# Optimization experiments

Hardware: AMD Instinct MI355X
Metric: run time of the kernel (lower is better)

Reference implementation:

```python
import jax, jax.numpy as jnp
import numpy as np
import math

B, T, D, H, L = 64, 255, 512, 8, 8
CODEBOOK = 512
V = CODEBOOK + 3  # bos/eos/pad
COND_DIM = 512
MAX_LEN = 256
HD = D // H


def _layernorm(x, g, b, eps=1e-5):
    mu = jnp.mean(x, axis=-1, keepdims=True)
    var = jnp.mean(jnp.square(x - mu), axis=-1, keepdims=True)
    return (x - mu) * jax.lax.rsqrt(var + eps) * g + b


def setup_inputs() -> dict:
    key = jax.random.key(0)
    ks = jax.random.split(key, 24)
    s = 0.02
    d = {
        'tokens': jax.random.randint(ks[0], (B, T), 0, V),
        'cond': jax.random.normal(ks[1], (B, COND_DIM), jnp.float32),
        'emb': jax.random.normal(ks[2], (V, D), jnp.float32) * s,  # tied token_emb / head weight
        'pos_emb': jax.random.normal(ks[3], (1, MAX_LEN, D), jnp.float32) * s,
        'cond_w1': jax.random.normal(ks[4], (COND_DIM, D), jnp.float32) * s,
        'cond_b1': jnp.zeros((D,), jnp.float32),
        'cond_w2': jax.random.normal(ks[5], (D, D), jnp.float32) * s,
        'cond_b2': jnp.zeros((D,), jnp.float32),
        'ln1_g': jnp.ones((L, D), jnp.float32),
        'ln1_b': jnp.zeros((L, D), jnp.float32),
        'qkv_w': jax.random.normal(ks[6], (L, D, 3 * D), jnp.float32) * s,
        'qkv_b': jnp.zeros((L, 3 * D), jnp.float32),
        'proj_w': jax.random.normal(ks[7], (L, D, D), jnp.float32) * s,
        'proj_b': jnp.zeros((L, D), jnp.float32),
        'ln2_g': jnp.ones((L, D), jnp.float32),
        'ln2_b': jnp.zeros((L, D), jnp.float32),
        'mlp_w1': jax.random.normal(ks[8], (L, D, 4 * D), jnp.float32) * s,
        'mlp_b1': jnp.zeros((L, 4 * D), jnp.float32),
        'mlp_w2': jax.random.normal(ks[9], (L, 4 * D, D), jnp.float32) * s,
        'mlp_b2': jnp.zeros((L, D), jnp.float32),
        'lnf_g': jnp.ones((D,), jnp.float32),
        'lnf_b': jnp.zeros((D,), jnp.float32),
    }
    return d


def reference(tokens, cond, emb, pos_emb, cond_w1, cond_b1, cond_w2, cond_b2,
              ln1_g, ln1_b, qkv_w, qkv_b, proj_w, proj_b,
              ln2_g, ln2_b, mlp_w1, mlp_b1, mlp_w2, mlp_b2, lnf_g, lnf_b):
    b, t = tokens.shape
    h = emb[tokens] + pos_emb[:, :t, :]                              # [B,T,D]
    c = jax.nn.silu(cond @ cond_w1 + cond_b1) @ cond_w2 + cond_b2    # [B,D]
    h = jnp.concatenate([c[:, None, :], h], axis=1)                  # [B,S,D]
    S = t + 1
    causal = jnp.tril(jnp.ones((S, S), bool))
    scale = 1.0 / math.sqrt(HD)
    for i in range(L):
        x = _layernorm(h, ln1_g[i], ln1_b[i])
        qkv = (x @ qkv_w[i] + qkv_b[i]).reshape(b, S, 3, H, HD).transpose(2, 0, 3, 1, 4)
        q, k, v = qkv[0], qkv[1], qkv[2]                             # [B,H,S,hd]
        a = jnp.einsum('bhsd,bhtd->bhst', q, k) * scale
        a = jnp.where(causal, a, -jnp.inf)
        a = jax.nn.softmax(a, axis=-1)
        o = jnp.einsum('bhst,bhtd->bhsd', a, v).transpose(0, 2, 1, 3).reshape(b, S, D)
        h = h + o @ proj_w[i] + proj_b[i]
        x = _layernorm(h, ln2_g[i], ln2_b[i])
        h = h + jax.nn.gelu(x @ mlp_w1[i] + mlp_b1[i], approximate=False) @ mlp_w2[i] + mlp_b2[i]
    h = _layernorm(h, lnf_g, lnf_b)
    return (h @ emb.T)[:, 1:, :]                                     # [B,T,V]
```

## Files before the change

kernel.cpp:

```cpp
#include <hip/hip_runtime.h>
#include <hip/hip_bf16.h>

typedef __attribute__((ext_vector_type(8))) short bf16x8;
typedef __attribute__((ext_vector_type(4))) float f32x4;
typedef __attribute__((ext_vector_type(4))) unsigned short u16x4;
typedef __attribute__((ext_vector_type(8))) unsigned short u16x8;
typedef unsigned short u16;

#define DEV static __device__ __forceinline__

DEV float bf2f(u16 u) {
  union { unsigned int i; float f; } c; c.i = ((unsigned int)u) << 16; return c.f;
}
DEV u16 f2bf(float f) {
  union { float f; unsigned int i; } c; c.f = f;
  unsigned int i = c.i;
  i += 0x7FFFu + ((i >> 16) & 1u);
  return (u16)(i >> 16);
}

DEV void gload_lds16(const void* g, void* l) {
  __builtin_amdgcn_global_load_lds((const __attribute__((address_space(1))) void*)g,
                                   (__attribute__((address_space(3))) void*)l, 16, 0, 0);
}

DEV f32x4 mfma16(bf16x8 a, bf16x8 b, f32x4 c) {
  return __builtin_amdgcn_mfma_f32_16x16x32_bf16(a, b, c, 0, 0, 0);
}

template<int N> DEV void vwait() { asm volatile("s_waitcnt vmcnt(%0)" :: "n"(N) : "memory"); }

DEV float gelu(float x) {
  float t2 = __builtin_fmaf(0.044715f * x * x, x, x);
  float e = __expf(1.5957691216f * t2);
  float th = 1.f - 2.f / (e + 1.f);
  return 0.5f * x * (1.f + th);
}

__global__ __launch_bounds__(256) void ktranspose(const float* __restrict__ in, u16* __restrict__ out,
                                                  int K, int N) {
  __shared__ u16 tile[32][33];
  const float* src = in + (size_t)blockIdx.z * K * N;
  u16* dst = out + (size_t)blockIdx.z * K * N;
  const int n0 = blockIdx.x * 32, k0 = blockIdx.y * 32;
  const int tx = threadIdx.x, ty = threadIdx.y;
#pragma unroll
  for (int i = ty; i < 32; i += 8) tile[i][tx] = f2bf(src[(size_t)(k0 + i) * N + n0 + tx]);
  __syncthreads();
#pragma unroll
  for (int i = ty; i < 32; i += 8) dst[(size_t)(n0 + i) * K + k0 + tx] = tile[tx][i];
}

__global__ __launch_bounds__(256) void kcvt(const float* __restrict__ in, u16* __restrict__ out, int n) {
  int i = blockIdx.x * 256 + threadIdx.x;
  if (i < n) out[i] = f2bf(in[i]);
}

__global__ __launch_bounds__(256) void kcond(const float* __restrict__ cond, const float* __restrict__ w1,
                                             const float* __restrict__ b1, const float* __restrict__ w2,
                                             const float* __restrict__ b2, float* __restrict__ h) {
  __shared__ float xr[512];
  __shared__ float t1[512];
  const int b = blockIdx.x, tid = threadIdx.x;
  for (int i = tid; i < 512; i += 256) xr[i] = cond[b * 512 + i];
  __syncthreads();
  for (int j = tid; j < 512; j += 256) {
    float acc = b1[j];
    for (int k = 0; k < 512; ++k) acc += xr[k] * w1[k * 512 + j];
    t1[j] = acc / (1.f + __expf(-acc));
  }
  __syncthreads();
  for (int j = tid; j < 512; j += 256) {
    float acc = b2[j];
    for (int k = 0; k < 512; ++k) acc += t1[k] * w2[k * 512 + j];
    h[(size_t)b * 256 * 512 + j] = acc;
  }
}

__global__ __launch_bounds__(256) void kembed(const int* __restrict__ tok, const float* __restrict__ emb,
                                              const float* __restrict__ pos, float* __restrict__ h) {
  const int idx = blockIdx.x;
  const int b = idx / 255, t = idx % 255;
  const int c = threadIdx.x * 2;
  const int tk = tok[idx];
  float2 ev = *(const float2*)(emb + (size_t)tk * 512 + c);
  float2 pv = *(const float2*)(pos + (size_t)t * 512 + c);
  float2 r;
  r.x = ev.x + pv.x;
  r.y = ev.y + pv.y;
  *(float2*)(h + ((size_t)b * 256 + 1 + t) * 512 + c) = r;
}

__global__ __launch_bounds__(256) void kln(const float* __restrict__ hin, const float* __restrict__ g,
                                           const float* __restrict__ bt, u16* __restrict__ out) {
  const int row = blockIdx.x * 4 + (threadIdx.x >> 6), lane = threadIdx.x & 63;
  const float4* x = (const float4*)(hin + (size_t)row * 512);
  float4 v0 = x[lane], v1 = x[lane + 64];
  float s1 = v0.x + v0.y + v0.z + v0.w + v1.x + v1.y + v1.z + v1.w;
  float s2 = v0.x * v0.x + v0.y * v0.y + v0.z * v0.z + v0.w * v0.w +
             v1.x * v1.x + v1.y * v1.y + v1.z * v1.z + v1.w * v1.w;
#pragma unroll
  for (int off = 1; off < 64; off <<= 1) { s1 += __shfl_xor(s1, off); s2 += __shfl_xor(s2, off); }
  float mu = s1 * (1.f / 512.f);
  float var = s2 * (1.f / 512.f) - mu * mu;
  float rs = rsqrtf(var + 1e-5f);
  const int c0 = lane * 4;
  float4 g0 = *(const float4*)(g + c0), g1 = *(const float4*)(g + 256 + c0);
  float4 b0 = *(const float4*)(bt + c0), b1 = *(const float4*)(bt + 256 + c0);
  u16x4 o0, o1;
  o0[0] = f2bf((v0.x - mu) * rs * g0.x + b0.x);
  o0[1] = f2bf((v0.y - mu) * rs * g0.y + b0.y);
  o0[2] = f2bf((v0.z - mu) * rs * g0.z + b0.z);
  o0[3] = f2bf((v0.w - mu) * rs * g0.w + b0.w);
  o1[0] = f2bf((v1.x - mu) * rs * g1.x + b1.x);
  o1[1] = f2bf((v1.y - mu) * rs * g1.y + b1.y);
  o1[2] = f2bf((v1.z - mu) * rs * g1.z + b1.z);
  o1[3] = f2bf((v1.w - mu) * rs * g1.w + b1.w);
  *(u16x4*)(out + (size_t)row * 512 + c0) = o0;
  *(u16x4*)(out + (size_t)row * 512 + 256 + c0) = o1;
}

template<int MODE>
__global__ __launch_bounds__(256, 2) void kgemm3(const u16* __restrict__ A, const u16* __restrict__ Bt,
                                                 const float* __restrict__ bias, void* __restrict__ Cout,
                                                 int M, int N, int K) {
  __shared__ __align__(16) u16 As[3][4096];
  __shared__ __align__(16) u16 Bs[3][4096];
  const int tid = threadIdx.x;
  const int lane = tid & 63;
  const int wr = tid >> 7, wc = (tid >> 6) & 1;
  const int m0 = blockIdx.x * 128, n0 = blockIdx.y * 128;
  const int nkt = K >> 5;
  const size_t Kb = (size_t)K * 2;

  const int srow = tid >> 2;
  const int schunk = tid & 3;
  const int sc = schunk ^ ((srow >> 1) & 3);
  const int d1 = tid * 16, d2 = tid * 16 + 4096;
  int brA = n0 + srow, brB = n0 + srow + 64;
  if (MODE == 3) { brA = min(brA, N - 1); brB = min(brB, N - 1); }
  const char* Ab = (const char*)A;
  const char* Bb = (const char*)Bt;
  const size_t a0 = (size_t)(m0 + srow) * Kb + sc * 16;
  const size_t a1 = (size_t)(m0 + srow + 64) * Kb + sc * 16;
  const size_t b0 = (size_t)brA * Kb + sc * 16;
  const size_t b1 = (size_t)brB * Kb + sc * 16;

  f32x4 acc[4][4];
#pragma unroll
  for (int i = 0; i < 4; ++i)
#pragma unroll
    for (int j = 0; j < 4; ++j) acc[i][j] = f32x4{0.f, 0.f, 0.f, 0.f};

#pragma unroll
  for (int t = 0; t < 2; ++t) {
    const size_t ko = (size_t)t * 64;
    gload_lds16(Ab + a0 + ko, (char*)As[t] + d1);
    gload_lds16(Ab + a1 + ko, (char*)As[t] + d2);
    gload_lds16(Bb + b0 + ko, (char*)Bs[t] + d1);
    gload_lds16(Bb + b1 + ko, (char*)Bs[t] + d2);
  }
  asm volatile("s_waitcnt vmcnt(4)" ::: "memory");
  __builtin_amdgcn_s_barrier();
  __builtin_amdgcn_sched_barrier(0);

  const int kchunk = (((lane >> 4) ^ ((lane >> 1) & 3)) << 4);
  const int arow = wr * 64 + (lane & 15);
  const int brow = wc * 64 + (lane & 15);

  for (int kt = 0; kt < nkt; ++kt) {
    const int bufc = kt % 3;
    const bool deep = (kt + 2 < nkt);
    if (deep) {
      const int bufn = (kt + 2) % 3;
      const size_t ko = (size_t)(kt + 2) * 64;
      gload_lds16(Ab + a0 + ko, (char*)As[bufn] + d1);
      gload_lds16(Ab + a1 + ko, (char*)As[bufn] + d2);
      gload_lds16(Bb + b0 + ko, (char*)Bs[bufn] + d1);
      gload_lds16(Bb + b1 + ko, (char*)Bs[bufn] + d2);
    }
    const char* Ap = (const char*)As[bufc];
    const char* Bp = (const char*)Bs[bufc];
    bf16x8 aF[4], bF[4];
#pragma unroll
    for (int mt = 0; mt < 4; ++mt) aF[mt] = *(const bf16x8*)(Ap + (arow + mt * 16) * 64 + kchunk);
#pragma unroll
    for (int nt = 0; nt < 4; ++nt) bF[nt] = *(const bf16x8*)(Bp + (brow + nt * 16) * 64 + kchunk);
#pragma unroll
    for (int mt = 0; mt < 4; ++mt)
#pragma unroll
      for (int nt = 0; nt < 4; ++nt)
        acc[mt][nt] = mfma16(aF[mt], bF[nt], acc[mt][nt]);
    if (deep) {
      asm volatile("s_waitcnt vmcnt(4)" ::: "memory");
    } else {
      asm volatile("s_waitcnt vmcnt(0)" ::: "memory");
    }
    __builtin_amdgcn_s_barrier();
    __builtin_amdgcn_sched_barrier(0);
  }

  float bv[4];
#pragma unroll
  for (int nt = 0; nt < 4; ++nt) {
    int col = n0 + wc * 64 + nt * 16 + (lane & 15);
    bv[nt] = (MODE == 3) ? 0.f : bias[col];
  }

  if (MODE == 0 || MODE == 1) {
    u16* C = (u16*)Cout;
#pragma unroll
    for (int mt = 0; mt < 4; ++mt)
#pragma unroll
      for (int r = 0; r < 4; ++r) {
        int row = m0 + wr * 64 + mt * 16 + (lane >> 4) * 4 + r;
        u16* cp = C + (size_t)row * N + n0 + wc * 64 + (lane & 15);
#pragma unroll
        for (int nt = 0; nt < 4; ++nt) {
          float v = acc[mt][nt][r] + bv[nt];
          if (MODE == 1) v = gelu(v);
          cp[nt * 16] = f2bf(v);
        }
      }
  } else if (MODE == 2) {
    float* hC = (float*)Cout;
#pragma unroll
    for (int mt = 0; mt < 4; ++mt)
#pragma unroll
      for (int r = 0; r < 4; ++r) {
        int row = m0 + wr * 64 + mt * 16 + (lane >> 4) * 4 + r;
        float* hp = hC + (size_t)row * N + n0 + wc * 64 + (lane & 15);
#pragma unroll
        for (int nt = 0; nt < 4; ++nt) hp[nt * 16] += acc[mt][nt][r] + bv[nt];
      }
  } else {
    float* C = (float*)Cout;
#pragma unroll
    for (int mt = 0; mt < 4; ++mt)
#pragma unroll
      for (int r = 0; r < 4; ++r) {
        int row = m0 + wr * 64 + mt * 16 + (lane >> 4) * 4 + r;
        int s = row & 255;
        if (s == 0) continue;
        int bb = row >> 8;
        float* cp = C + ((size_t)bb * 255 + (s - 1)) * 515 + n0 + wc * 64 + (lane & 15);
#pragma unroll
        for (int nt = 0; nt < 4; ++nt) {
          int col = n0 + wc * 64 + nt * 16 + (lane & 15);
          if (col < 515) cp[nt * 16] = acc[mt][nt][r];
        }
      }
  }
}

template<int MODE, int FM>
__global__ __launch_bounds__(512, 2) void kgemm8(const u16* __restrict__ A, const u16* __restrict__ Bt,
                                                 const float* __restrict__ bias, void* __restrict__ Cout,
                                                 int M, int N, int K) {
  constexpr int BM = FM * 32;
  constexpr int ABYTES = BM * 128;
  constexpr int BBYTES = 256 * 128;
  constexpr int AH = ABYTES / 2, BH = BBYTES / 2;
  constexpr int ALD = AH / 8192;
  constexpr int BOFF = 2 * ABYTES;
  __shared__ __align__(16) char shm[2 * ABYTES + 2 * BBYTES];

  const int tid = threadIdx.x;
  const int lane = tid & 63;
  const int wid = tid >> 6;
  const int wr = wid >> 2;
  const int wc = wid & 3;
  const int fr = lane & 15, fq = lane >> 4;
  const int axor = (fr & 7) << 4;
  const int m0 = blockIdx.x * BM, n0 = blockIdx.y * 256;
  const int nkt = K >> 6;
  const int Kb = K * 2;
  const char* Ab = (const char*)A;
  const char* Bb = (const char*)Bt;

  unsigned aOff[2][ALD], bOff[2][2];
#pragma unroll
  for (int h = 0; h < 2; ++h) {
#pragma unroll
    for (int j = 0; j < ALD; ++j) {
      int d = h * AH + j * 8192 + tid * 16;
      int row = d >> 7, pc = (d >> 4) & 7;
      aOff[h][j] = (unsigned)((m0 + row) * Kb + ((pc ^ (row & 7)) << 4));
    }
#pragma unroll
    for (int j = 0; j < 2; ++j) {
      int d = h * BH + j * 8192 + tid * 16;
      int row = d >> 7, pc = (d >> 4) & 7;
      bOff[h][j] = (unsigned)((n0 + row) * Kb + ((pc ^ (row & 7)) << 4));
    }
  }

  auto stA = [&](int kt, int h, int b) {
#pragma unroll
    for (int j = 0; j < ALD; ++j)
      gload_lds16(Ab + (size_t)aOff[h][j] + (size_t)kt * 128,
                  shm + b * ABYTES + h * AH + j * 8192 + tid * 16);
  };
  auto stB = [&](int kt, int h, int b) {
#pragma unroll
    for (int j = 0; j < 2; ++j)
      gload_lds16(Bb + (size_t)bOff[h][j] + (size_t)kt * 128,
                  shm + BOFF + b * BBYTES + h * BH + j * 8192 + tid * 16);
  };
  auto rdA = [&](int b, int m, int ks) {
    return *(const bf16x8*)(shm + b * ABYTES + (wr * (BM / 2) + m * 16 + fr) * 128 +
                            ((ks * 64 + fq * 16) ^ axor));
  };
  auto rdB = [&](int b, int n, int ks) {
    return *(const bf16x8*)(shm + BOFF + b * BBYTES + (wc * 64 + n * 16 + fr) * 128 +
                            ((ks * 64 + fq * 16) ^ axor));
  };

  f32x4 acc[FM][4];
#pragma unroll
  for (int i = 0; i < FM; ++i)
#pragma unroll
    for (int j = 0; j < 4; ++j) acc[i][j] = f32x4{0.f, 0.f, 0.f, 0.f};

  stA(0, 0, 0); stA(0, 1, 0); stB(0, 0, 0); stB(0, 1, 0);
  if (nkt > 1) { stA(1, 0, 1); stA(1, 1, 1); }
  vwait<2 * ALD>();
  __builtin_amdgcn_sched_barrier(0);
  __builtin_amdgcn_s_barrier();

  for (int kt = 0; kt < nkt; ++kt) {
    const int cur = kt & 1;
    const bool sb = (kt + 1 < nkt);
    const bool sa = (kt + 2 < nkt);
    bf16x8 aF[FM][2], bF[4][2];
#pragma unroll
    for (int m = 0; m < FM; ++m) aF[m][0] = rdA(cur, m, 0);
#pragma unroll
    for (int n = 0; n < 4; ++n) bF[n][0] = rdB(cur, n, 0);
    if (sb) stB(kt + 1, 0, cur ^ 1);
    __builtin_amdgcn_s_barrier();
    __builtin_amdgcn_s_setprio(1);
#pragma unroll
    for (int m = 0; m < FM / 2; ++m)
#pragma unroll
      for (int n = 0; n < 4; ++n) acc[m][n] = mfma16(aF[m][0], bF[n][0], acc[m][n]);
    __builtin_amdgcn_s_setprio(0);
    __builtin_amdgcn_s_barrier();
#pragma unroll
    for (int m = 0; m < FM; ++m) aF[m][1] = rdA(cur, m, 1);
#pragma unroll
    for (int n = 0; n < 4; ++n) bF[n][1] = rdB(cur, n, 1);
    if (sb) stB(kt + 1, 1, cur ^ 1);
    __builtin_amdgcn_s_barrier();
    __builtin_amdgcn_s_setprio(1);
#pragma unroll
    for (int m = FM / 2; m < FM; ++m)
#pragma unroll
      for (int n = 0; n < 4; ++n) acc[m][n] = mfma16(aF[m][0], bF[n][0], acc[m][n]);
    __builtin_amdgcn_s_setprio(0);
    asm volatile("s_waitcnt lgkmcnt(0)" ::: "memory");
    __builtin_amdgcn_sched_barrier(0);
    __builtin_amdgcn_s_barrier();
    if (sa) stA(kt + 2, 0, cur);
    __builtin_amdgcn_s_barrier();
    __builtin_amdgcn_s_setprio(1);
#pragma unroll
    for (int m = 0; m < FM / 2; ++m)
#pragma unroll
      for (int n = 0; n < 4; ++n) acc[m][n] = mfma16(aF[m][1], bF[n][1], acc[m][n]);
    __builtin_amdgcn_s_setprio(0);
    __builtin_amdgcn_s_barrier();
    if (sa) stA(kt + 2, 1, cur);
    __builtin_amdgcn_s_barrier();
    __builtin_amdgcn_s_setprio(1);
#pragma unroll
    for (int m = FM / 2; m < FM; ++m)
#pragma unroll
      for (int n = 0; n < 4; ++n) acc[m][n] = mfma16(aF[m][1], bF[n][1], acc[m][n]);
    __builtin_amdgcn_s_setprio(0);
    if (sa) vwait<2 * ALD>(); else vwait<0>();
    __builtin_amdgcn_sched_barrier(0);
    __builtin_amdgcn_s_barrier();
  }

  float bv[4];
#pragma unroll
  for (int n = 0; n < 4; ++n) bv[n] = bias[n0 + wc * 64 + n * 16 + fr];

  float* hC = (float*)Cout;
#pragma unroll
  for (int m = 0; m < FM; ++m)
#pragma unroll
    for (int r = 0; r < 4; ++r) {
      int row = m0 + wr * (BM / 2) + m * 16 + fq * 4 + r;
      float* hp = hC + (size_t)row * N + n0 + wc * 64 + fr;
#pragma unroll
      for (int n = 0; n < 4; ++n) hp[n * 16] += acc[m][n][r] + bv[n];
    }
}

__global__ __launch_bounds__(256, 1) void kattn(const u16* __restrict__ qkv, u16* __restrict__ o) {
  __shared__ __align__(16) u16 Ks[256][72];
  __shared__ __align__(16) u16 Vt[64][264];
  __shared__ __align__(16) u16 Ps[4][64][72];
  const int tid = threadIdx.x, wv = tid >> 6, lane = tid & 63;
  const int bh = blockIdx.x, bb = bh >> 3, hh = bh & 7;
  const size_t base = (size_t)bb * 256 * 1536 + hh * 64;

  for (int c = tid; c < 2048; c += 256) {
    int s = c >> 3, pp = c & 7;
    u16x8 kv = *(const u16x8*)(qkv + base + (size_t)s * 1536 + 512 + pp * 8);
    *(u16x8*)&Ks[s][pp * 8] = kv;
    u16x8 vv = *(const u16x8*)(qkv + base + (size_t)s * 1536 + 1024 + pp * 8);
#pragma unroll
    for (int j = 0; j < 8; ++j) Vt[pp * 8 + j][s] = vv[j];
  }
  __syncthreads();

  bf16x8 qf[4][2];
#pragma unroll
  for (int mt = 0; mt < 4; ++mt)
#pragma unroll
    for (int ks = 0; ks < 2; ++ks)
      qf[mt][ks] = *(const bf16x8*)(qkv + base +
                   (size_t)(wv * 64 + mt * 16 + (lane & 15)) * 1536 + ks * 32 + (lane >> 4) * 8);

  const float scale = 0.125f;
  float mrow[4][4], lsum[4][4];
#pragma unroll
  for (int mt = 0; mt < 4; ++mt)
#pragma unroll
    for (int r = 0; r < 4; ++r) { mrow[mt][r] = -1e30f; lsum[mt][r] = 0.f; }

  f32x4 oacc[4][4];
#pragma unroll
  for (int i = 0; i < 4; ++i)
#pragma unroll
    for (int j = 0; j < 4; ++j) oacc[i][j] = f32x4{0.f, 0.f, 0.f, 0.f};

  for (int ct = 0; ct <= wv; ++ct) {
    f32x4 sacc[4][4];
#pragma unroll
    for (int i = 0; i < 4; ++i)
#pragma unroll
      for (int j = 0; j < 4; ++j) sacc[i][j] = f32x4{0.f, 0.f, 0.f, 0.f};
#pragma unroll
    for (int ks = 0; ks < 2; ++ks) {
      bf16x8 kf[4];
#pragma unroll
      for (int nt = 0; nt < 4; ++nt)
        kf[nt] = *(const bf16x8*)&Ks[ct * 64 + nt * 16 + (lane & 15)][ks * 32 + (lane >> 4) * 8];
#pragma unroll
      for (int mt = 0; mt < 4; ++mt)
#pragma unroll
        for (int nt = 0; nt < 4; ++nt)
          sacc[mt][nt] = mfma16(qf[mt][ks], kf[nt], sacc[mt][nt]);
    }
#pragma unroll
    for (int mt = 0; mt < 4; ++mt)
#pragma unroll
      for (int r = 0; r < 4; ++r) {
        int srow = wv * 64 + mt * 16 + (lane >> 4) * 4 + r;
        float v[4];
        float mx = -1e30f;
#pragma unroll
        for (int nt = 0; nt < 4; ++nt) {
          int tcol = ct * 64 + nt * 16 + (lane & 15);
          float vv = sacc[mt][nt][r] * scale;
          v[nt] = (tcol > srow) ? -1e30f : vv;
          mx = fmaxf(mx, v[nt]);
        }
#pragma unroll
        for (int off = 1; off < 16; off <<= 1) mx = fmaxf(mx, __shfl_xor(mx, off));
        float mnew = fmaxf(mrow[mt][r], mx);
        float sf = __expf(mrow[mt][r] - mnew);
        mrow[mt][r] = mnew;
        float ps = 0.f;
#pragma unroll
        for (int nt = 0; nt < 4; ++nt) {
          float pe = (v[nt] <= -1e29f) ? 0.f : __expf(v[nt] - mnew);
          ps += pe;
          Ps[wv][mt * 16 + (lane >> 4) * 4 + r][nt * 16 + (lane & 15)] = f2bf(pe);
        }
#pragma unroll
        for (int off = 1; off < 16; off <<= 1) ps += __shfl_xor(ps, off);
        lsum[mt][r] = lsum[mt][r] * sf + ps;
#pragma unroll
        for (int nt = 0; nt < 4; ++nt) oacc[mt][nt][r] *= sf;
      }
#pragma unroll
    for (int ks = 0; ks < 2; ++ks) {
      bf16x8 pf[4], vf[4];
#pragma unroll
      for (int mt = 0; mt < 4; ++mt)
        pf[mt] = *(const bf16x8*)&Ps[wv][mt * 16 + (lane & 15)][ks * 32 + (lane >> 4) * 8];
#pragma unroll
      for (int nt = 0; nt < 4; ++nt)
        vf[nt] = *(const bf16x8*)&Vt[nt * 16 + (lane & 15)][ct * 64 + ks * 32 + (lane >> 4) * 8];
#pragma unroll
      for (int mt = 0; mt < 4; ++mt)
#pragma unroll
        for (int nt = 0; nt < 4; ++nt)
          oacc[mt][nt] = mfma16(pf[mt], vf[nt], oacc[mt][nt]);
    }
  }

#pragma unroll
  for (int mt = 0; mt < 4; ++mt)
#pragma unroll
    for (int r = 0; r < 4; ++r) {
      int s = wv * 64 + mt * 16 + (lane >> 4) * 4 + r;
      float inv = 1.f / lsum[mt][r];
      u16* op = o + ((size_t)bb * 256 + s) * 512 + hh * 64 + (lane & 15);
#pragma unroll
      for (int nt = 0; nt < 4; ++nt) op[nt * 16] = f2bf(oacc[mt][nt][r] * inv);
    }
}

extern "C" void kernel_launch(void* const* d_in, const int* in_sizes, int n_in,
                              void* d_out, int out_size, void* d_ws, size_t ws_size,
                              hipStream_t stream) {
  const int* tokens = (const int*)d_in[0];
  const float* cond = (const float*)d_in[1];
  const float* emb = (const float*)d_in[2];
  const float* pos = (const float*)d_in[3];
  const float* cw1 = (const float*)d_in[4];
  const float* cb1 = (const float*)d_in[5];
  const float* cw2 = (const float*)d_in[6];
  const float* cb2 = (const float*)d_in[7];
  const float* ln1g = (const float*)d_in[8];
  const float* ln1b = (const float*)d_in[9];
  const float* qkvw = (const float*)d_in[10];
  const float* qkvb = (const float*)d_in[11];
  const float* projw = (const float*)d_in[12];
  const float* projb = (const float*)d_in[13];
  const float* ln2g = (const float*)d_in[14];
  const float* ln2b = (const float*)d_in[15];
  const float* w1 = (const float*)d_in[16];
  const float* b1 = (const float*)d_in[17];
  const float* w2 = (const float*)d_in[18];
  const float* b2 = (const float*)d_in[19];
  const float* lnfg = (const float*)d_in[20];
  const float* lnfb = (const float*)d_in[21];

  const size_t NEEDED = (size_t)16384 * 512 * 4
                      + (size_t)16384 * 512 * 2
                      + (size_t)16384 * 2048 * 2
                      + (size_t)8 * 1536 * 512 * 2
                      + (size_t)8 * 512 * 512 * 2
                      + (size_t)8 * 2048 * 512 * 2
                      + (size_t)8 * 512 * 2048 * 2;
  if (ws_size < NEEDED) return;

  char* p = (char*)d_ws;
  float* h = (float*)p;        p += (size_t)16384 * 512 * 4;
  u16* xln = (u16*)p;          p += (size_t)16384 * 512 * 2;
  u16* big = (u16*)p;          p += (size_t)16384 * 2048 * 2;
  u16* attn_o = big + (size_t)16384 * 1536;
  u16* embB = big;
  u16* qkvT = (u16*)p;         p += (size_t)8 * 1536 * 512 * 2;
  u16* projT = (u16*)p;        p += (size_t)8 * 512 * 512 * 2;
  u16* w1T = (u16*)p;          p += (size_t)8 * 2048 * 512 * 2;
  u16* w2T = (u16*)p;          p += (size_t)8 * 512 * 2048 * 2;

  ktranspose<<<dim3(48, 16, 8), dim3(32, 8), 0, stream>>>(qkvw, qkvT, 512, 1536);
  ktranspose<<<dim3(16, 16, 8), dim3(32, 8), 0, stream>>>(projw, projT, 512, 512);
  ktranspose<<<dim3(64, 16, 8), dim3(32, 8), 0, stream>>>(w1, w1T, 512, 2048);
  ktranspose<<<dim3(16, 64, 8), dim3(32, 8), 0, stream>>>(w2, w2T, 2048, 512);

  kembed<<<16320, 256, 0, stream>>>(tokens, emb, pos, h);
  kcond<<<64, 256, 0, stream>>>(cond, cw1, cb1, cw2, cb2, h);

  for (int l = 0; l < 8; ++l) {
    kln<<<4096, 256, 0, stream>>>(h, ln1g + l * 512, ln1b + l * 512, xln);
    kgemm3<0><<<dim3(128, 12), 256, 0, stream>>>(xln, qkvT + (size_t)l * 1536 * 512,
                                                 qkvb + l * 1536, big, 16384, 1536, 512);
    kattn<<<512, 256, 0, stream>>>(big, attn_o);
    kgemm8<2, 4><<<dim3(128, 2), 512, 0, stream>>>(attn_o, projT + (size_t)l * 512 * 512,
                                                   projb + l * 512, h, 16384, 512, 512);
    kln<<<4096, 256, 0, stream>>>(h, ln2g + l * 512, ln2b + l * 512, xln);
    kgemm3<1><<<dim3(128, 16), 256, 0, stream>>>(xln, w1T + (size_t)l * 2048 * 512,
                                                 b1 + l * 2048, big, 16384, 2048, 512);
    kgemm8<2, 4><<<dim3(128, 2), 512, 0, stream>>>(big, w2T + (size_t)l * 512 * 2048,
                                                   b2 + l * 512, h, 16384, 512, 2048);
  }
  kln<<<4096, 256, 0, stream>>>(h, lnfg, lnfb, xln);
  kcvt<<<1030, 256, 0, stream>>>(emb, embB, 515 * 512);
  kgemm3<3><<<dim3(128, 5), 256, 0, stream>>>(xln, embB, nullptr, d_out, 16384, 515, 512);
}
```

Baseline: 1.985 ms.

## Store residual stream in bf16 instead of fp32

Changes the residual hidden-state buffer from fp32 to bf16 across embedding, cond, layernorm and the projection/MLP-down GEMM epilogues. Layernorm now reads 8 bf16 values per lane, and the GEMM epilogue reads, adds and rewrites bf16. This halves the memory traffic for residual reads and read-modify-writes. The trade-off is that residual accumulation across layers happens in bf16, reducing numerical accuracy.

```diff
diff --git a/kernel.cpp b/kernel.cpp
--- a/kernel.cpp
+++ b/kernel.cpp
@@ -3,6 +3,7 @@
 
 typedef __attribute__((ext_vector_type(8))) short bf16x8;
 typedef __attribute__((ext_vector_type(4))) float f32x4;
+typedef __attribute__((ext_vector_type(2))) unsigned short u16x2;
 typedef __attribute__((ext_vector_type(4))) unsigned short u16x4;
 typedef __attribute__((ext_vector_type(8))) unsigned short u16x8;
 typedef unsigned short u16;
@@ -58,7 +59,7 @@
 
 __global__ __launch_bounds__(256) void kcond(const float* __restrict__ cond, const float* __restrict__ w1,
                                              const float* __restrict__ b1, const float* __restrict__ w2,
-                                             const float* __restrict__ b2, float* __restrict__ h) {
+                                             const float* __restrict__ b2, u16* __restrict__ h) {
   __shared__ float xr[512];
   __shared__ float t1[512];
   const int b = blockIdx.x, tid = threadIdx.x;
@@ -73,51 +74,54 @@
   for (int j = tid; j < 512; j += 256) {
     float acc = b2[j];
     for (int k = 0; k < 512; ++k) acc += t1[k] * w2[k * 512 + j];
-    h[(size_t)b * 256 * 512 + j] = acc;
+    h[(size_t)b * 256 * 512 + j] = f2bf(acc);
   }
 }
 
 __global__ __launch_bounds__(256) void kembed(const int* __restrict__ tok, const float* __restrict__ emb,
-                                              const float* __restrict__ pos, float* __restrict__ h) {
+                                              const float* __restrict__ pos, u16* __restrict__ h) {
   const int idx = blockIdx.x;
   const int b = idx / 255, t = idx % 255;
   const int c = threadIdx.x * 2;
   const int tk = tok[idx];
   float2 ev = *(const float2*)(emb + (size_t)tk * 512 + c);
   float2 pv = *(const float2*)(pos + (size_t)t * 512 + c);
-  float2 r;
-  r.x = ev.x + pv.x;
-  r.y = ev.y + pv.y;
-  *(float2*)(h + ((size_t)b * 256 + 1 + t) * 512 + c) = r;
-}
-
-__global__ __launch_bounds__(256) void kln(const float* __restrict__ hin, const float* __restrict__ g,
+  u16x2 r;
+  r[0] = f2bf(ev.x + pv.x);
+  r[1] = f2bf(ev.y + pv.y);
+  *(u16x2*)(h + ((size_t)b * 256 + 1 + t) * 512 + c) = r;
+}
+
+__global__ __launch_bounds__(256) void kln(const u16* __restrict__ hin, const float* __restrict__ g,
                                            const float* __restrict__ bt, u16* __restrict__ out) {
   const int row = blockIdx.x * 4 + (threadIdx.x >> 6), lane = threadIdx.x & 63;
-  const float4* x = (const float4*)(hin + (size_t)row * 512);
-  float4 v0 = x[lane], v1 = x[lane + 64];
-  float s1 = v0.x + v0.y + v0.z + v0.w + v1.x + v1.y + v1.z + v1.w;
-  float s2 = v0.x * v0.x + v0.y * v0.y + v0.z * v0.z + v0.w * v0.w +
-             v1.x * v1.x + v1.y * v1.y + v1.z * v1.z + v1.w * v1.w;
+  u16x8 xv = *(const u16x8*)(hin + (size_t)row * 512 + lane * 8);
+  float x[8];
+  float s1 = 0.f, s2 = 0.f;
+#pragma unroll
+  for (int j = 0; j < 8; ++j) {
+    x[j] = bf2f(xv[j]);
+    s1 += x[j];
+    s2 += x[j] * x[j];
+  }
 #pragma unroll
   for (int off = 1; off < 64; off <<= 1) { s1 += __shfl_xor(s1, off); s2 += __shfl_xor(s2, off); }
   float mu = s1 * (1.f / 512.f);
   float var = s2 * (1.f / 512.f) - mu * mu;
   float rs = rsqrtf(var + 1e-5f);
-  const int c0 = lane * 4;
-  float4 g0 = *(const float4*)(g + c0), g1 = *(const float4*)(g + 256 + c0);
-  float4 b0 = *(const float4*)(bt + c0), b1 = *(const float4*)(bt + 256 + c0);
-  u16x4 o0, o1;
-  o0[0] = f2bf((v0.x - mu) * rs * g0.x + b0.x);
-  o0[1] = f2bf((v0.y - mu) * rs * g0.y + b0.y);
-  o0[2] = f2bf((v0.z - mu) * rs * g0.z + b0.z);
-  o0[3] = f2bf((v0.w - mu) * rs * g0.w + b0.w);
-  o1[0] = f2bf((v1.x - mu) * rs * g1.x + b1.x);
-  o1[1] = f2bf((v1.y - mu) * rs * g1.y + b1.y);
-  o1[2] = f2bf((v1.z - mu) * rs * g1.z + b1.z);
-  o1[3] = f2bf((v1.w - mu) * rs * g1.w + b1.w);
-  *(u16x4*)(out + (size_t)row * 512 + c0) = o0;
-  *(u16x4*)(out + (size_t)row * 512 + 256 + c0) = o1;
+  const int c0 = lane * 8;
+  float4 g0 = *(const float4*)(g + c0), g1 = *(const float4*)(g + c0 + 4);
+  float4 b0 = *(const float4*)(bt + c0), b1 = *(const float4*)(bt + c0 + 4);
+  u16x8 o;
+  o[0] = f2bf((x[0] - mu) * rs * g0.x + b0.x);
+  o[1] = f2bf((x[1] - mu) * rs * g0.y + b0.y);
+  o[2] = f2bf((x[2] - mu) * rs * g0.z + b0.z);
+  o[3] = f2bf((x[3] - mu) * rs * g0.w + b0.w);
+  o[4] = f2bf((x[4] - mu) * rs * g1.x + b1.x);
+  o[5] = f2bf((x[5] - mu) * rs * g1.y + b1.y);
+  o[6] = f2bf((x[6] - mu) * rs * g1.z + b1.z);
+  o[7] = f2bf((x[7] - mu) * rs * g1.w + b1.w);
+  *(u16x8*)(out + (size_t)row * 512 + c0) = o;
 }
 
 template<int MODE>
@@ -222,17 +226,6 @@
           cp[nt * 16] = f2bf(v);
         }
       }
-  } else if (MODE == 2) {
-    float* hC = (float*)Cout;
-#pragma unroll
-    for (int mt = 0; mt < 4; ++mt)
-#pragma unroll
-      for (int r = 0; r < 4; ++r) {
-        int row = m0 + wr * 64 + mt * 16 + (lane >> 4) * 4 + r;
-        float* hp = hC + (size_t)row * N + n0 + wc * 64 + (lane & 15);
-#pragma unroll
-        for (int nt = 0; nt < 4; ++nt) hp[nt * 16] += acc[mt][nt][r] + bv[nt];
-      }
   } else {
     float* C = (float*)Cout;
 #pragma unroll
@@ -253,16 +246,16 @@
   }
 }
 
-template<int MODE, int FM>
+template<int FM>
 __global__ __launch_bounds__(512, 2) void kgemm8(const u16* __restrict__ A, const u16* __restrict__ Bt,
-                                                 const float* __restrict__ bias, void* __restrict__ Cout,
+                                                 const float* __restrict__ bias, u16* __restrict__ h,
                                                  int M, int N, int K) {
-  constexpr int BM = FM * 32;
-  constexpr int ABYTES = BM * 128;
+  constexpr int ABYTES = FM * 32 * 128;
   constexpr int BBYTES = 256 * 128;
   constexpr int AH = ABYTES / 2, BH = BBYTES / 2;
   constexpr int ALD = AH / 8192;
   constexpr int BOFF = 2 * ABYTES;
+  constexpr int BM = FM * 32;
   __shared__ __align__(16) char shm[2 * ABYTES + 2 * BBYTES];
 
   const int tid = threadIdx.x;
@@ -280,32 +273,32 @@
 
   unsigned aOff[2][ALD], bOff[2][2];
 #pragma unroll
-  for (int h = 0; h < 2; ++h) {
+  for (int hh = 0; hh < 2; ++hh) {
 #pragma unroll
     for (int j = 0; j < ALD; ++j) {
-      int d = h * AH + j * 8192 + tid * 16;
+      int d = hh * AH + j * 8192 + tid * 16;
       int row = d >> 7, pc = (d >> 4) & 7;
-      aOff[h][j] = (unsigned)((m0 + row) * Kb + ((pc ^ (row & 7)) << 4));
+      aOff[hh][j] = (unsigned)((m0 + row) * Kb + ((pc ^ (row & 7)) << 4));
     }
 #pragma unroll
     for (int j = 0; j < 2; ++j) {
-      int d = h * BH + j * 8192 + tid * 16;
+      int d = hh * BH + j * 8192 + tid * 16;
       int row = d >> 7, pc = (d >> 4) & 7;
-      bOff[h][j] = (unsigned)((n0 + row) * Kb + ((pc ^ (row & 7)) << 4));
-    }
-  }
-
-  auto stA = [&](int kt, int h, int b) {
+      bOff[hh][j] = (unsigned)((n0 + row) * Kb + ((pc ^ (row & 7)) << 4));
+    }
+  }
+
+  auto stA = [&](int kt, int hh, int b) {
 #pragma unroll
     for (int j = 0; j < ALD; ++j)
-      gload_lds16(Ab + (size_t)aOff[h][j] + (size_t)kt * 128,
-                  shm + b * ABYTES + h * AH + j * 8192 + tid * 16);
+      gload_lds16(Ab + (size_t)aOff[hh][j] + (size_t)kt * 128,
+                  shm + b * ABYTES + hh * AH + j * 8192 + tid * 16);
   };
-  auto stB = [&](int kt, int h, int b) {
+  auto stB = [&](int kt, int hh, int b) {
 #pragma unroll
     for (int j = 0; j < 2; ++j)
-      gload_lds16(Bb + (size_t)bOff[h][j] + (size_t)kt * 128,
-                  shm + BOFF + b * BBYTES + h * BH + j * 8192 + tid * 16);
+      gload_lds16(Bb + (size_t)bOff[hh][j] + (size_t)kt * 128,
+                  shm + BOFF + b * BBYTES + hh * BH + j * 8192 + tid * 16);
   };
   auto rdA = [&](int b, int m, int ks) {
     return *(const bf16x8*)(shm + b * ABYTES + (wr * (BM / 2) + m * 16 + fr) * 128 +
@@ -387,15 +380,17 @@
 #pragma unroll
   for (int n = 0; n < 4; ++n) bv[n] = bias[n0 + wc * 64 + n * 16 + fr];
 
-  float* hC = (float*)Cout;
 #pragma unroll
   for (int m = 0; m < FM; ++m)
 #pragma unroll
     for (int r = 0; r < 4; ++r) {
       int row = m0 + wr * (BM / 2) + m * 16 + fq * 4 + r;
-      float* hp = hC + (size_t)row * N + n0 + wc * 64 + fr;
-#pragma unroll
-      for (int n = 0; n < 4; ++n) hp[n * 16] += acc[m][n][r] + bv[n];
+      u16* hp = h + (size_t)row * N + n0 + wc * 64 + fr;
+#pragma unroll
+      for (int n = 0; n < 4; ++n) {
+        float val = acc[m][n][r] + bv[n] + bf2f(hp[n * 16]);
+        hp[n * 16] = f2bf(val);
+      }
     }
 }
 
@@ -543,7 +538,7 @@
   const float* lnfg = (const float*)d_in[20];
   const float* lnfb = (const float*)d_in[21];
 
-  const size_t NEEDED = (size_t)16384 * 512 * 4
+  const size_t NEEDED = (size_t)16384 * 512 * 2
                       + (size_t)16384 * 512 * 2
                       + (size_t)16384 * 2048 * 2
                       + (size_t)8 * 1536 * 512 * 2
@@ -553,7 +548,7 @@
   if (ws_size < NEEDED) return;
 
   char* p = (char*)d_ws;
-  float* h = (float*)p;        p += (size_t)16384 * 512 * 4;
+  u16* h = (u16*)p;            p += (size_t)16384 * 512 * 2;
   u16* xln = (u16*)p;          p += (size_t)16384 * 512 * 2;
   u16* big = (u16*)p;          p += (size_t)16384 * 2048 * 2;
   u16* attn_o = big + (size_t)16384 * 1536;
@@ -576,13 +571,13 @@
     kgemm3<0><<<dim3(128, 12), 256, 0, stream>>>(xln, qkvT + (size_t)l * 1536 * 512,
                                                  qkvb + l * 1536, big, 16384, 1536, 512);
     kattn<<<512, 256, 0, stream>>>(big, attn_o);
-    kgemm8<2, 4><<<dim3(128, 2), 512, 0, stream>>>(attn_o, projT + (size_t)l * 512 * 512,
-                                                   projb + l * 512, h, 16384, 512, 512);
+    kgemm8<4><<<dim3(128, 2), 512, 0, stream>>>(attn_o, projT + (size_t)l * 512 * 512,
+                                                projb + l * 512, h, 16384, 512, 512);
     kln<<<4096, 256, 0, stream>>>(h, ln2g + l * 512, ln2b + l * 512, xln);
     kgemm3<1><<<dim3(128, 16), 256, 0, stream>>>(xln, w1T + (size_t)l * 2048 * 512,
                                                  b1 + l * 2048, big, 16384, 2048, 512);
-    kgemm8<2, 4><<<dim3(128, 2), 512, 0, stream>>>(big, w2T + (size_t)l * 512 * 2048,
-                                                   b2 + l * 512, h, 16384, 512, 2048);
+    kgemm8<4><<<dim3(128, 2), 512, 0, stream>>>(big, w2T + (size_t)l * 512 * 2048,
+                                                b2 + l * 512, h, 16384, 512, 2048);
   }
   kln<<<4096, 256, 0, stream>>>(h, lnfg, lnfb, xln);
   kcvt<<<1030, 256, 0, stream>>>(emb, embB, 515 * 512);
```

After: 1.878 ms. 5.4% less time.
